# Kernel tuning notes

Hardware: AMD Instinct MI355X
Metric: run time of the kernel (lower is better)

The kernel has to match this reference:

```python
import jax, jax.numpy as jnp
import numpy as np


def _pool_mat(n_in, n_out):
    # AdaptiveAvgPool1d(n_out) over a length-n_in axis, as a dense [n_out, n_in] averaging matrix.
    M = np.zeros((n_out, n_in), dtype=np.float32)
    for i in range(n_out):
        s = (i * n_in) // n_out
        e = -(-((i + 1) * n_in) // n_out)  # ceil
        M[i, s:e] = 1.0 / (e - s)
    return M


def _ln(x, g, b, eps=1e-5):
    m = jnp.mean(x, axis=-1, keepdims=True)
    xc = x - m
    v = jnp.mean(xc * xc, axis=-1, keepdims=True)
    return xc * jax.lax.rsqrt(v + eps) * g + b


def setup_inputs():
    T, TOK, P, N, D, L, C = 16, 16384, 8192, 32768, 128, 8, 16
    key = jax.random.key(0)
    ks = jax.random.split(key, 9)
    x = jax.random.normal(ks[0], (T, TOK, D), dtype=jnp.float32)
    # P node-token positions per timestamp (models padded_node_mask with P True entries)
    node_pos = jnp.sort(jax.vmap(lambda k: jax.random.permutation(k, TOK)[:P])(jax.random.split(ks[1], T)), axis=1).astype(jnp.int32)
    # unique entire-graph node ids per timestamp (scatter destinations)
    node_ids = jax.vmap(lambda k: jax.random.permutation(k, N)[:P])(jax.random.split(ks[2], T)).astype(jnp.int32)
    g_enc = 1.0 + 0.1 * jax.random.normal(ks[3], (D,), dtype=jnp.float32)
    b_enc = 0.1 * jax.random.normal(ks[4], (D,), dtype=jnp.float32)
    g_fin = 1.0 + 0.1 * jax.random.normal(ks[5], (L * C,), dtype=jnp.float32)
    b_fin = 0.1 * jax.random.normal(ks[6], (L * C,), dtype=jnp.float32)
    g_dec = 1.0 + 0.1 * jax.random.normal(ks[7], (C,), dtype=jnp.float32)
    b_dec = 0.1 * jax.random.normal(ks[8], (C,), dtype=jnp.float32)
    return {"x": x, "g_enc": g_enc, "b_enc": b_enc, "g_fin": g_fin, "b_fin": b_fin,
            "g_dec": g_dec, "b_dec": b_dec, "node_pos": node_pos, "node_ids": node_ids,
            "num_nodes": N}


def reference(x, g_enc, b_enc, g_fin, b_fin, g_dec, b_dec, node_pos, node_ids, num_nodes):
    T, TOK, D = x.shape
    C = g_dec.shape[0]
    L = g_fin.shape[0] // C
    N = int(num_nodes)
    # ---- encode ----
    xn = _ln(x, g_enc, b_enc)                                   # encode_layer_norm
    nodes = jnp.take_along_axis(xn, node_pos[:, :, None], axis=1)  # masked gather [T,P,D]
    # _to_entire: scatter node embeddings into zero [T,N,D]
    tee = jnp.zeros((T, N, D), x.dtype).at[jnp.arange(T)[:, None], node_ids].set(nodes)
    A1 = jnp.asarray(_pool_mat(D, C))                            # AdaptiveAvgPool1d(comp_dim)
    pooled = jnp.einsum('tnd,cd->tnc', tee, A1)                  # [T,N,C]
    groups = np.array_split(np.arange(N), L)
    max_len = max(len(g) for g in groups)
    stacked = np.stack([np.pad(g, (0, max_len - len(g))) for g in groups])  # [L,max_len]
    grouped = jnp.take(pooled, jnp.asarray(stacked), axis=1)     # [T,L,max_len,C]
    comp = (grouped.sum(axis=2) / max_len).reshape(T, 1, L * C)  # segment mean-pool
    comp = _ln(comp, g_fin, b_fin)                               # encode_final_layer_norm
    # ---- decode ----
    vals = jnp.broadcast_to(comp.reshape(T, L, 1, C), (T, L, max_len, C)).reshape(T, L * max_len, C)
    tee2 = jnp.zeros((T, N, C), x.dtype).at[:, jnp.asarray(stacked.reshape(-1)), :].set(vals)
    dn = _ln(tee2, g_dec, b_dec)                                 # decode_norm
    A2 = jnp.asarray(_pool_mat(C, D))                            # AdaptiveAvgPool1d(embed_dim)
    out = jnp.einsum('tnc,dc->tnd', dn, A2)                      # [T,N,D]
    return out
```

## Files before the change

### kernel.cpp

```cpp
#include <hip/hip_runtime.h>

#define T_   16
#define TOK_ 16384
#define P_   8192
#define N_   32768
#define D_   128
#define L_   8
#define C_   16

typedef float f32x4 __attribute__((ext_vector_type(4)));

constexpr int K1_BLOCKS     = 1024;
constexpr int BLOCKS_PER_T  = 64;
constexpr int K3_BLOCKS     = 512;

__global__ __launch_bounds__(256) void k1_gather_ln_pool(
    const float* __restrict__ x,
    const float* __restrict__ g_enc, const float* __restrict__ b_enc,
    const int* __restrict__ node_pos, const int* __restrict__ node_ids,
    float* __restrict__ partial)
{
    __shared__ float lds[4 * 128];
    const int tid   = threadIdx.x;
    const int lane  = tid & 63;
    const int wid   = tid >> 6;
    const int j     = lane & 15;
    const int q     = lane >> 4;
    const int b     = blockIdx.x;
    const int t     = b >> 6;
    const int chunk = b & 63;
    const int tP    = t * P_;
    const float* xt = x + (size_t)t * TOK_ * D_;

    const f32x4 g0  = *(const f32x4*)(g_enc + 8 * j);
    const f32x4 g1  = *(const f32x4*)(g_enc + 8 * j + 4);
    const f32x4 bb0 = *(const f32x4*)(b_enc + 8 * j);
    const f32x4 bb1 = *(const f32x4*)(b_enc + 8 * j + 4);
    const float G = g0.x + g0.y + g0.z + g0.w + g1.x + g1.y + g1.z + g1.w;
    const float B = bb0.x + bb0.y + bb0.z + bb0.w + bb1.x + bb1.y + bb1.z + bb1.w;

    float acc[L_];
#pragma unroll
    for (int ll = 0; ll < L_; ++ll) acc[ll] = 0.f;

#pragma unroll
    for (int pass = 0; pass < 2; ++pass) {
        const int pbase = chunk * 128 + pass * 64 + wid * 16;
        const int posv = node_pos[tP + pbase + j];
        const int nidv = node_ids[tP + pbase + j];

        f32x4 va[4], vb[4];
#pragma unroll
        for (int i = 0; i < 4; ++i) {
            const int p = __shfl(posv, i * 4 + q);
            const float* row = xt + (size_t)p * D_ + 8 * j;
            va[i] = *(const f32x4*)(row);
            vb[i] = *(const f32x4*)(row + 4);
        }
#pragma unroll
        for (int i = 0; i < 4; ++i) {
            const f32x4 a = va[i], c = vb[i];
            float s  = a.x + a.y + a.z + a.w + c.x + c.y + c.z + c.w;
            float ss = a.x*a.x + a.y*a.y + a.z*a.z + a.w*a.w
                     + c.x*c.x + c.y*c.y + c.z*c.z + c.w*c.w;
            float dot = a.x*g0.x + a.y*g0.y + a.z*g0.z + a.w*g0.w
                      + c.x*g1.x + c.y*g1.y + c.z*g1.z + c.w*g1.w;
#pragma unroll
            for (int m = 1; m < 16; m <<= 1) {
                s  += __shfl_xor(s, m);
                ss += __shfl_xor(ss, m);
            }
            const float mean = s * (1.f / 128.f);
            const float rstd = rsqrtf(ss * (1.f / 128.f) - mean * mean + 1e-5f);
            const float srow = (dot - mean * G) * rstd + B;
            const int l = __shfl(nidv, i * 4 + q) >> 12;
#pragma unroll
            for (int ll = 0; ll < L_; ++ll) acc[ll] += (ll == l) ? srow : 0.f;
        }
    }

#pragma unroll
    for (int ll = 0; ll < L_; ++ll) {
        acc[ll] += __shfl_xor(acc[ll], 16);
        acc[ll] += __shfl_xor(acc[ll], 32);
    }
    if (lane < 16) {
#pragma unroll
        for (int ll = 0; ll < L_; ++ll) lds[wid * 128 + ll * 16 + j] = acc[ll];
    }
    __syncthreads();
    if (tid < 128) {
        const float sum = lds[tid] + lds[128 + tid] + lds[256 + tid] + lds[384 + tid];
        partial[(size_t)b * 128 + tid] = sum;
    }
}

__global__ __launch_bounds__(64) void k2_finalize(
    const float* __restrict__ partial,
    const float* __restrict__ g_fin, const float* __restrict__ b_fin,
    const float* __restrict__ g_dec, const float* __restrict__ b_dec,
    float* __restrict__ decoded)
{
    const int t = blockIdx.x;
    const int lane = threadIdx.x;
    const float* pb = partial + (size_t)t * BLOCKS_PER_T * 128;
    float a0 = 0.f, a1 = 0.f;
#pragma unroll 8
    for (int k = 0; k < BLOCKS_PER_T; ++k) {
        a0 += pb[k * 128 + lane];
        a1 += pb[k * 128 + 64 + lane];
    }
    a0 *= (1.f / 32768.f);
    a1 *= (1.f / 32768.f);

    float s = a0 + a1, ss = a0 * a0 + a1 * a1;
#pragma unroll
    for (int m = 1; m < 64; m <<= 1) {
        s  += __shfl_xor(s, m);
        ss += __shfl_xor(ss, m);
    }
    const float mean = s * (1.f / 128.f);
    const float rstd = rsqrtf(ss * (1.f / 128.f) - mean * mean + 1e-5f);
    const float c0 = (a0 - mean) * rstd * g_fin[lane]      + b_fin[lane];
    const float c1 = (a1 - mean) * rstd * g_fin[lane + 64] + b_fin[lane + 64];

    float s0 = c0, q0 = c0 * c0, s1 = c1, q1 = c1 * c1;
#pragma unroll
    for (int m = 1; m < 16; m <<= 1) {
        s0 += __shfl_xor(s0, m); q0 += __shfl_xor(q0, m);
        s1 += __shfl_xor(s1, m); q1 += __shfl_xor(q1, m);
    }
    const float m0 = s0 * (1.f / 16.f), m1 = s1 * (1.f / 16.f);
    const float r0 = rsqrtf(q0 * (1.f / 16.f) - m0 * m0 + 1e-5f);
    const float r1 = rsqrtf(q1 * (1.f / 16.f) - m1 * m1 + 1e-5f);
    const int c = lane & 15;
    const float gd = g_dec[c], bd = b_dec[c];
    decoded[t * 128 + lane]      = (c0 - m0) * r0 * gd + bd;
    decoded[t * 128 + 64 + lane] = (c1 - m1) * r1 * gd + bd;
}

__global__ __launch_bounds__(256) void k3_broadcast(
    const float* __restrict__ decoded, f32x4* __restrict__ out)
{
    const int tid  = threadIdx.x;
    const int lane = tid & 63;
    const int wid  = tid >> 6;
    const int b    = blockIdx.x;
    const int t    = b >> 5;
    const int s    = b & 31;
    const int l    = s >> 2;
    const float val = decoded[(t << 7) + (l << 4) + ((lane & 31) >> 1)];
    const f32x4 v4 = {val, val, val, val};
    f32x4* p = out + (((size_t)t << 20) + ((size_t)s << 15) + (wid << 13) + lane);
#pragma unroll 8
    for (int it = 0; it < 128; ++it)
        __builtin_nontemporal_store(v4, p + (it << 6));
}

extern "C" void kernel_launch(void* const* d_in, const int* in_sizes, int n_in,
                              void* d_out, int out_size, void* d_ws, size_t ws_size,
                              hipStream_t stream)
{
    const float* x      = (const float*)d_in[0];
    const float* g_enc  = (const float*)d_in[1];
    const float* b_enc  = (const float*)d_in[2];
    const float* g_fin  = (const float*)d_in[3];
    const float* b_fin  = (const float*)d_in[4];
    const float* g_dec  = (const float*)d_in[5];
    const float* b_dec  = (const float*)d_in[6];
    const int*   node_pos = (const int*)d_in[7];
    const int*   node_ids = (const int*)d_in[8];

    float* partial = (float*)d_ws;
    float* decoded = partial + (size_t)K1_BLOCKS * 128;
    float* out = (float*)d_out;

    hipLaunchKernelGGL(k1_gather_ln_pool, dim3(K1_BLOCKS), dim3(256), 0, stream,
                       x, g_enc, b_enc, node_pos, node_ids, partial);
    hipLaunchKernelGGL(k2_finalize, dim3(T_), dim3(64), 0, stream,
                       partial, g_fin, b_fin, g_dec, b_dec, decoded);
    hipLaunchKernelGGL(k3_broadcast, dim3(K3_BLOCKS), dim3(256), 0, stream,
                       decoded, (f32x4*)out);
}
```

Measured before the change: 70.88 us.

## Fuse finalize into broadcast kernel and hoist all gather loads in k1

Drops the separate single-wave-per-timestamp finalize kernel. Each broadcast block now redundantly reduces the 64 partial rows for its timestamp, applies both layer norms in LDS, and then streams out the output, which removes one launch and its serialization gap. In k1, the index loads and all eight row loads per wave are issued up front across both passes so more memory requests are in flight. The cost is redundant finalize work in 32 blocks per timestamp, plus higher register pressure from holding 16 vectors.

```diff
diff --git a/kernel.cpp b/kernel.cpp
--- a/kernel.cpp
+++ b/kernel.cpp
@@ -30,6 +30,7 @@
     const int t     = b >> 6;
     const int chunk = b & 63;
     const int tP    = t * P_;
+    const int pbase = chunk * 128 + wid * 16;
     const float* xt = x + (size_t)t * TOK_ * D_;
 
     const f32x4 g0  = *(const f32x4*)(g_enc + 8 * j);
@@ -39,27 +40,33 @@
     const float G = g0.x + g0.y + g0.z + g0.w + g1.x + g1.y + g1.z + g1.w;
     const float B = bb0.x + bb0.y + bb0.z + bb0.w + bb1.x + bb1.y + bb1.z + bb1.w;
 
+    int posv[2], nidv[2];
+    posv[0] = node_pos[tP + pbase + j];
+    nidv[0] = node_ids[tP + pbase + j];
+    posv[1] = node_pos[tP + pbase + 64 + j];
+    nidv[1] = node_ids[tP + pbase + 64 + j];
+
+    f32x4 va[8], vb[8];
+#pragma unroll
+    for (int pass = 0; pass < 2; ++pass) {
+#pragma unroll
+        for (int i = 0; i < 4; ++i) {
+            const int p = __shfl(posv[pass], i * 4 + q);
+            const float* row = xt + (size_t)p * D_ + 8 * j;
+            va[pass * 4 + i] = *(const f32x4*)(row);
+            vb[pass * 4 + i] = *(const f32x4*)(row + 4);
+        }
+    }
+
     float acc[L_];
 #pragma unroll
     for (int ll = 0; ll < L_; ++ll) acc[ll] = 0.f;
 
 #pragma unroll
     for (int pass = 0; pass < 2; ++pass) {
-        const int pbase = chunk * 128 + pass * 64 + wid * 16;
-        const int posv = node_pos[tP + pbase + j];
-        const int nidv = node_ids[tP + pbase + j];
-
-        f32x4 va[4], vb[4];
 #pragma unroll
         for (int i = 0; i < 4; ++i) {
-            const int p = __shfl(posv, i * 4 + q);
-            const float* row = xt + (size_t)p * D_ + 8 * j;
-            va[i] = *(const f32x4*)(row);
-            vb[i] = *(const f32x4*)(row + 4);
-        }
-#pragma unroll
-        for (int i = 0; i < 4; ++i) {
-            const f32x4 a = va[i], c = vb[i];
+            const f32x4 a = va[pass * 4 + i], c = vb[pass * 4 + i];
             float s  = a.x + a.y + a.z + a.w + c.x + c.y + c.z + c.w;
             float ss = a.x*a.x + a.y*a.y + a.z*a.z + a.w*a.w
                      + c.x*c.x + c.y*c.y + c.z*c.z + c.w*c.w;
@@ -73,7 +80,7 @@
             const float mean = s * (1.f / 128.f);
             const float rstd = rsqrtf(ss * (1.f / 128.f) - mean * mean + 1e-5f);
             const float srow = (dot - mean * G) * rstd + B;
-            const int l = __shfl(nidv, i * 4 + q) >> 12;
+            const int l = __shfl(nidv[pass], i * 4 + q) >> 12;
 #pragma unroll
             for (int ll = 0; ll < L_; ++ll) acc[ll] += (ll == l) ? srow : 0.f;
         }
@@ -95,61 +102,63 @@
     }
 }
 
-__global__ __launch_bounds__(64) void k2_finalize(
+__global__ __launch_bounds__(256) void k3_finalize_broadcast(
     const float* __restrict__ partial,
     const float* __restrict__ g_fin, const float* __restrict__ b_fin,
     const float* __restrict__ g_dec, const float* __restrict__ b_dec,
-    float* __restrict__ decoded)
+    f32x4* __restrict__ out)
 {
-    const int t = blockIdx.x;
-    const int lane = threadIdx.x;
-    const float* pb = partial + (size_t)t * BLOCKS_PER_T * 128;
-    float a0 = 0.f, a1 = 0.f;
-#pragma unroll 8
-    for (int k = 0; k < BLOCKS_PER_T; ++k) {
-        a0 += pb[k * 128 + lane];
-        a1 += pb[k * 128 + 64 + lane];
-    }
-    a0 *= (1.f / 32768.f);
-    a1 *= (1.f / 32768.f);
-
-    float s = a0 + a1, ss = a0 * a0 + a1 * a1;
-#pragma unroll
-    for (int m = 1; m < 64; m <<= 1) {
-        s  += __shfl_xor(s, m);
-        ss += __shfl_xor(ss, m);
-    }
-    const float mean = s * (1.f / 128.f);
-    const float rstd = rsqrtf(ss * (1.f / 128.f) - mean * mean + 1e-5f);
-    const float c0 = (a0 - mean) * rstd * g_fin[lane]      + b_fin[lane];
-    const float c1 = (a1 - mean) * rstd * g_fin[lane + 64] + b_fin[lane + 64];
-
-    float s0 = c0, q0 = c0 * c0, s1 = c1, q1 = c1 * c1;
-#pragma unroll
-    for (int m = 1; m < 16; m <<= 1) {
-        s0 += __shfl_xor(s0, m); q0 += __shfl_xor(q0, m);
-        s1 += __shfl_xor(s1, m); q1 += __shfl_xor(q1, m);
-    }
-    const float m0 = s0 * (1.f / 16.f), m1 = s1 * (1.f / 16.f);
-    const float r0 = rsqrtf(q0 * (1.f / 16.f) - m0 * m0 + 1e-5f);
-    const float r1 = rsqrtf(q1 * (1.f / 16.f) - m1 * m1 + 1e-5f);
-    const int c = lane & 15;
-    const float gd = g_dec[c], bd = b_dec[c];
-    decoded[t * 128 + lane]      = (c0 - m0) * r0 * gd + bd;
-    decoded[t * 128 + 64 + lane] = (c1 - m1) * r1 * gd + bd;
-}
-
-__global__ __launch_bounds__(256) void k3_broadcast(
-    const float* __restrict__ decoded, f32x4* __restrict__ out)
-{
+    __shared__ float hsum[2][128];
+    __shared__ float dec[128];
     const int tid  = threadIdx.x;
     const int lane = tid & 63;
     const int wid  = tid >> 6;
     const int b    = blockIdx.x;
     const int t    = b >> 5;
     const int s    = b & 31;
-    const int l    = s >> 2;
-    const float val = decoded[(t << 7) + (l << 4) + ((lane & 31) >> 1)];
+
+    {
+        const float* pb = partial + (size_t)t * BLOCKS_PER_T * 128;
+        const int ch = tid & 127, h = tid >> 7;
+        float a = 0.f;
+#pragma unroll 8
+        for (int k = 0; k < 32; ++k)
+            a += pb[(h * 32 + k) * 128 + ch];
+        hsum[h][ch] = a;
+        __syncthreads();
+        if (wid == 0) {
+            float c0 = (hsum[0][lane] + hsum[1][lane]) * (1.f / 32768.f);
+            float c1 = (hsum[0][64 + lane] + hsum[1][64 + lane]) * (1.f / 32768.f);
+            float sm = c0 + c1, ss = c0 * c0 + c1 * c1;
+#pragma unroll
+            for (int m = 1; m < 64; m <<= 1) {
+                sm += __shfl_xor(sm, m);
+                ss += __shfl_xor(ss, m);
+            }
+            const float mean = sm * (1.f / 128.f);
+            const float rstd = rsqrtf(ss * (1.f / 128.f) - mean * mean + 1e-5f);
+            const float e0 = (c0 - mean) * rstd * g_fin[lane]      + b_fin[lane];
+            const float e1 = (c1 - mean) * rstd * g_fin[lane + 64] + b_fin[lane + 64];
+
+            float s0 = e0, q0 = e0 * e0, s1 = e1, q1 = e1 * e1;
+#pragma unroll
+            for (int m = 1; m < 16; m <<= 1) {
+                s0 += __shfl_xor(s0, m); q0 += __shfl_xor(q0, m);
+                s1 += __shfl_xor(s1, m); q1 += __shfl_xor(q1, m);
+            }
+            const float m0 = s0 * (1.f / 16.f), m1 = s1 * (1.f / 16.f);
+            const float r0 = rsqrtf(q0 * (1.f / 16.f) - m0 * m0 + 1e-5f);
+            const float r1 = rsqrtf(q1 * (1.f / 16.f) - m1 * m1 + 1e-5f);
+            const int c = lane & 15;
+            const float gd = g_dec[c], bd = b_dec[c];
+            dec[lane]      = (e0 - m0) * r0 * gd + bd;
+            dec[64 + lane] = (e1 - m1) * r1 * gd + bd;
+        }
+        __syncthreads();
+    }
+
+    const int l = s >> 2;
+    const float val = dec[(l << 4) + ((lane & 31) >> 1)];
     const f32x4 v4 = {val, val, val, val};
     f32x4* p = out + (((size_t)t << 20) + ((size_t)s << 15) + (wid << 13) + lane);
 #pragma unroll 8
@@ -172,13 +181,10 @@
     const int*   node_ids = (const int*)d_in[8];
 
     float* partial = (float*)d_ws;
-    float* decoded = partial + (size_t)K1_BLOCKS * 128;
-    float* out = (float*)d_out;
+    float* out     = (float*)d_out;
 
     hipLaunchKernelGGL(k1_gather_ln_pool, dim3(K1_BLOCKS), dim3(256), 0, stream,
                        x, g_enc, b_enc, node_pos, node_ids, partial);
-    hipLaunchKernelGGL(k2_finalize, dim3(T_), dim3(64), 0, stream,
-                       partial, g_fin, b_fin, g_dec, b_dec, decoded);
-    hipLaunchKernelGGL(k3_broadcast, dim3(K3_BLOCKS), dim3(256), 0, stream,
-                       decoded, (f32x4*)out);
+    hipLaunchKernelGGL(k3_finalize_broadcast, dim3(K3_BLOCKS), dim3(256), 0, stream,
+                       partial, g_fin, b_fin, g_dec, b_dec, (f32x4*)out);
 }
```

New measurement: 68.53 us, median of 2. -3.3%, faster.
